# Kernel optimization log

Measured on AMD Instinct MI355X. Metric: run time of the kernel, lower is better.

## Reference

```python
import jax, jax.numpy as jnp
import numpy as np

N_NODES = 50000
N_EDGES = 800000
IN_CH = 512
HIDDEN = 512


def setup_inputs() -> dict:
    key = jax.random.key(0)
    k1, k2, k3, k4 = jax.random.split(key, 4)
    x = jax.random.normal(k1, (N_NODES, IN_CH), dtype=jnp.float32)
    edge_index = jax.random.randint(k2, (2, N_EDGES), 0, N_NODES, dtype=jnp.int64)
    # Glorot-style scaling for weights
    W1 = jax.random.normal(k3, (IN_CH, HIDDEN), dtype=jnp.float32) / np.sqrt(IN_CH)
    b1 = jnp.zeros((HIDDEN,), dtype=jnp.float32)
    W2 = jax.random.normal(k4, (HIDDEN, 1), dtype=jnp.float32) / np.sqrt(HIDDEN)
    b2 = jnp.zeros((1,), dtype=jnp.float32)
    return {"x": x, "edge_index": edge_index, "W1": W1, "b1": b1, "W2": W2, "b2": b2}


def _gcn_conv(x, edge_index, W, b):
    """PyG GCNConv: add self-loops, symmetric D^{-1/2}(A+I)D^{-1/2} normalization."""
    N = x.shape[0]
    xw = x @ W                                   # [N, out]
    row, col = edge_index[0], edge_index[1]      # source -> target
    # degree on target nodes, +1 for the self-loop
    deg = jax.ops.segment_sum(jnp.ones_like(col, dtype=xw.dtype), col, num_segments=N) + 1.0
    dis = jax.lax.rsqrt(deg)                     # deg^{-1/2}, [N]
    norm = dis[row] * dis[col]                   # [E]
    agg = jax.ops.segment_sum(norm[:, None] * xw[row], col, num_segments=N)
    agg = agg + (dis * dis)[:, None] * xw        # self-loop contribution
    return agg + b


def reference(x, edge_index, W1, b1, W2, b2):
    h = jax.nn.relu(_gcn_conv(x, edge_index, W1, b1))
    # dropout in eval mode (training=False) -> identity
    out = _gcn_conv(h, edge_index, W2, b2)
    return out.squeeze(-1)                       # [N]
```

## Files before the change

kernel.cpp:

```cpp
#include <hip/hip_runtime.h>

#define IN_CH 512
#define SCAN_BLK 1024

typedef _Float16 f16x8 __attribute__((ext_vector_type(8)));
typedef float f32x4 __attribute__((ext_vector_type(4)));

__device__ __forceinline__ void gload_lds16(const void* g, void* l) {
    __builtin_amdgcn_global_load_lds(
        (const __attribute__((address_space(1))) unsigned int*)g,
        (__attribute__((address_space(3))) unsigned int*)l, 16, 0, 0);
}

__global__ __launch_bounds__(256) void k_merged1(const float* __restrict__ W1,
                                                 _Float16* __restrict__ W1t,
                                                 const int* __restrict__ col,
                                                 int* __restrict__ deg, int E, int N) {
    __shared__ float tile[32][33];
    if ((int)blockIdx.x >= 256) {
        int e = ((int)blockIdx.x - 256) * 256 + threadIdx.x;
        if (e < E) {
            int d = col[e];
            if ((unsigned)d < (unsigned)N) atomicAdd(&deg[d], 1);
        }
        return;
    }
    const int bk = (blockIdx.x & 15) * 32, bn = (blockIdx.x >> 4) * 32;
    const int tx = threadIdx.x & 31, ty = threadIdx.x >> 5;
#pragma unroll
    for (int p = 0; p < 4; ++p)
        tile[ty + p * 8][tx] = W1[(size_t)(bk + ty + p * 8) * 512 + bn + tx];
    __syncthreads();
#pragma unroll
    for (int p = 0; p < 4; ++p)
        W1t[(size_t)(bn + ty + p * 8) * 512 + bk + tx] = (_Float16)tile[tx][ty + p * 8];
}

__global__ __launch_bounds__(SCAN_BLK) void k_psum(const int* __restrict__ deg,
                                                   int* __restrict__ bsum, int N) {
    __shared__ int red[SCAN_BLK / 64];
    int i = blockIdx.x * SCAN_BLK + threadIdx.x;
    int v = (i < N) ? deg[i] : 0;
#pragma unroll
    for (int off = 32; off > 0; off >>= 1) v += __shfl_down(v, off);
    if ((threadIdx.x & 63) == 0) red[threadIdx.x >> 6] = v;
    __syncthreads();
    if (threadIdx.x == 0) {
        int s = 0;
#pragma unroll
        for (int u = 0; u < SCAN_BLK / 64; ++u) s += red[u];
        bsum[blockIdx.x] = s;
    }
}

__global__ __launch_bounds__(SCAN_BLK) void k_write(const int* __restrict__ deg,
                                                    const int* __restrict__ bsum,
                                                    int* __restrict__ rp,
                                                    float* __restrict__ dis,
                                                    int* __restrict__ cursor, int N) {
    __shared__ int sums[SCAN_BLK];
    __shared__ int boff_s, tot_s;
    int t = threadIdx.x;
    if (t < 64) {
        int v = (t < (int)gridDim.x) ? bsum[t] : 0;
        int pre = (t < (int)blockIdx.x) ? v : 0;
        int a = pre, b = v;
#pragma unroll
        for (int off = 32; off > 0; off >>= 1) {
            a += __shfl_down(a, off);
            b += __shfl_down(b, off);
        }
        if (t == 0) { boff_s = a; tot_s = b; }
    }
    int i = blockIdx.x * SCAN_BLK + t;
    int d = (i < N) ? deg[i] : 0;
    sums[t] = d;
    __syncthreads();
    for (int off = 1; off < SCAN_BLK; off <<= 1) {
        int u = (t >= off) ? sums[t - off] : 0;
        __syncthreads();
        sums[t] += u;
        __syncthreads();
    }
    if (i < N) {
        rp[i] = boff_s + sums[t] - d;
        dis[i] = rsqrtf((float)d + 1.0f);
        cursor[i] = 0;
    }
    if (blockIdx.x == gridDim.x - 1 && t == 0) rp[N] = tot_s;
}

__global__ __launch_bounds__(256) void k_merged2(const float* __restrict__ A,
                                                 const _Float16* __restrict__ Bt,
                                                 _Float16* __restrict__ C,
                                                 int Nrows, int nbm, int nwg,
                                                 const int* __restrict__ ei,
                                                 const int* __restrict__ rp,
                                                 int* __restrict__ cursor,
                                                 int* __restrict__ csrc,
                                                 int E, int N) {
    __shared__ __align__(16) _Float16 As[128 * 64];
    __shared__ __align__(16) _Float16 Bs[128 * 64];

    if ((int)blockIdx.x >= nwg) {
        int e = ((int)blockIdx.x - nwg) * 256 + threadIdx.x;
        if (e < E) {
            int s = ei[e];
            int d = ei[E + e];
            if ((unsigned)s < (unsigned)N && (unsigned)d < (unsigned)N) {
                int pos = atomicAdd(&cursor[d], 1);
                csrc[rp[d] + pos] = s;
            }
        }
        return;
    }

    const int g = (int)blockIdx.x;
    const int t = threadIdx.x;
    const int lane = t & 63, w = t >> 6;
    const int wm = w >> 1, wn = w & 1;

    const int q = nwg >> 3, r = nwg & 7;
    const int xcd = g & 7, within = g >> 3;
    const int wg = (xcd < r ? xcd * (q + 1) : r * (q + 1) + (xcd - r) * q) + within;
    const int bm = (wg >> 2) * 128, bn = (wg & 3) * 128;

    const int rr = lane & 15, kg = lane >> 4;
    const int lrow = lane >> 3;
    const int scol = ((lane & 7) ^ lrow) * 8;
    const int rsw = rr & 7;
    const int arow = t >> 3;
    const int achk = t & 7;
    const int agcol = (achk ^ (arow & 7)) * 8;

    f32x4 acc[4][4];
#pragma unroll
    for (int i = 0; i < 4; ++i)
#pragma unroll
        for (int j = 0; j < 4; ++j) acc[i][j] = (f32x4)0.0f;

    for (int k0 = 0; k0 < 512; k0 += 64) {
#pragma unroll
        for (int p = 0; p < 4; ++p) {
            const int row = p * 32 + w * 8 + lrow;
            gload_lds16(Bt + (size_t)(bn + row) * 512 + k0 + scol,
                        Bs + (p * 32 + w * 8) * 64);
        }
#pragma unroll
        for (int p = 0; p < 4; ++p) {
            int grow = bm + p * 32 + arow;
            if (grow >= Nrows) grow = Nrows - 1;
            const float* gp = A + (size_t)grow * 512 + k0 + agcol;
            float4 u0 = *(const float4*)gp;
            float4 u1 = *(const float4*)(gp + 4);
            f16x8 o;
            o[0] = (_Float16)u0.x; o[1] = (_Float16)u0.y;
            o[2] = (_Float16)u0.z; o[3] = (_Float16)u0.w;
            o[4] = (_Float16)u1.x; o[5] = (_Float16)u1.y;
            o[6] = (_Float16)u1.z; o[7] = (_Float16)u1.w;
            *(f16x8*)(As + (p * 32 + arow) * 64 + achk * 8) = o;
        }
        __syncthreads();
#pragma unroll
        for (int kk = 0; kk < 2; ++kk) {
            f16x8 a[4], b[4];
#pragma unroll
            for (int i = 0; i < 4; ++i)
                a[i] = *(const f16x8*)(As + (wm * 64 + i * 16 + rr) * 64 +
                                       (((kk << 2) + kg) ^ rsw) * 8);
#pragma unroll
            for (int j = 0; j < 4; ++j)
                b[j] = *(const f16x8*)(Bs + (wn * 64 + j * 16 + rr) * 64 +
                                       (((kk << 2) + kg) ^ rsw) * 8);
#pragma unroll
            for (int i = 0; i < 4; ++i)
#pragma unroll
                for (int j = 0; j < 4; ++j)
                    acc[i][j] = __builtin_amdgcn_mfma_f32_16x16x32_f16(a[i], b[j], acc[i][j], 0, 0, 0);
        }
        __syncthreads();
    }

#pragma unroll
    for (int i = 0; i < 4; ++i)
#pragma unroll
        for (int j = 0; j < 4; ++j)
#pragma unroll
            for (int reg = 0; reg < 4; ++reg) {
                int m = bm + wm * 64 + i * 16 + kg * 4 + reg;
                int n = bn + wn * 64 + j * 16 + rr;
                C[(size_t)m * 512 + n] = (_Float16)acc[i][j][reg];
            }
}

__global__ __launch_bounds__(256) void k_agg(const _Float16* __restrict__ y,
                                             const float* __restrict__ dis,
                                             const int* __restrict__ rp,
                                             const int* __restrict__ csrc,
                                             const float* __restrict__ b1,
                                             const float* __restrict__ W2,
                                             float* __restrict__ z, int N) {
    const int n = blockIdx.x * 4 + (threadIdx.x >> 6);
    if (n >= N) return;
    const int l = threadIdx.x & 63;

    const float d1 = dis[n];
    f16x8 self = *(const f16x8*)(y + (size_t)n * 512 + l * 8);
    float acc[8];
#pragma unroll
    for (int c = 0; c < 8; ++c) acc[c] = d1 * (float)self[c];

    int j = rp[n], jend = rp[n + 1];
    for (; j + 8 <= jend; j += 8) {
        int s[8]; float wt[8]; f16x8 v[8];
#pragma unroll
        for (int u = 0; u < 8; ++u) s[u] = csrc[j + u];
#pragma unroll
        for (int u = 0; u < 8; ++u) wt[u] = dis[s[u]];
#pragma unroll
        for (int u = 0; u < 8; ++u)
            v[u] = *(const f16x8*)(y + (size_t)s[u] * 512 + l * 8);
#pragma unroll
        for (int u = 0; u < 8; ++u)
#pragma unroll
            for (int c = 0; c < 8; ++c) acc[c] += wt[u] * (float)v[u][c];
    }
    for (; j + 2 <= jend; j += 2) {
        int s0 = csrc[j], s1 = csrc[j + 1];
        float w0 = dis[s0], w1 = dis[s1];
        f16x8 v0 = *(const f16x8*)(y + (size_t)s0 * 512 + l * 8);
        f16x8 v1 = *(const f16x8*)(y + (size_t)s1 * 512 + l * 8);
#pragma unroll
        for (int c = 0; c < 8; ++c) acc[c] += w0 * (float)v0[c] + w1 * (float)v1[c];
    }
    if (j < jend) {
        int s0 = csrc[j];
        float w0 = dis[s0];
        f16x8 v0 = *(const f16x8*)(y + (size_t)s0 * 512 + l * 8);
#pragma unroll
        for (int c = 0; c < 8; ++c) acc[c] += w0 * (float)v0[c];
    }

    float4 bb0 = *(const float4*)(b1 + l * 8);
    float4 bb1 = *(const float4*)(b1 + l * 8 + 4);
    float4 w20 = *(const float4*)(W2 + l * 8);
    float4 w21 = *(const float4*)(W2 + l * 8 + 4);
    float bbv[8] = {bb0.x, bb0.y, bb0.z, bb0.w, bb1.x, bb1.y, bb1.z, bb1.w};
    float w2v[8] = {w20.x, w20.y, w20.z, w20.w, w21.x, w21.y, w21.z, w21.w};
    float p = 0.0f;
#pragma unroll
    for (int c = 0; c < 8; ++c) {
        float h = fmaxf(acc[c] * d1 + bbv[c], 0.0f);
        p += h * w2v[c];
    }
#pragma unroll
    for (int off = 32; off > 0; off >>= 1) p += __shfl_down(p, off);
    if (l == 0) z[n] = d1 * p;
}

__global__ void k_out(const float* __restrict__ z, const float* __restrict__ dis,
                      const int* __restrict__ rp, const int* __restrict__ csrc,
                      const float* __restrict__ b2, float* __restrict__ out, int N) {
    int n = blockIdx.x * blockDim.x + threadIdx.x;
    if (n >= N) return;
    float acc = z[n];
    int j = rp[n], jend = rp[n + 1];
    for (; j + 4 <= jend; j += 4) {
        float a0 = z[csrc[j]];
        float a1 = z[csrc[j + 1]];
        float a2 = z[csrc[j + 2]];
        float a3 = z[csrc[j + 3]];
        acc += (a0 + a1) + (a2 + a3);
    }
    for (; j < jend; ++j) acc += z[csrc[j]];
    out[n] = dis[n] * acc + b2[0];
}

extern "C" void kernel_launch(void* const* d_in, const int* in_sizes, int n_in,
                              void* d_out, int out_size, void* d_ws, size_t ws_size,
                              hipStream_t stream) {
    const float* x  = (const float*)d_in[0];
    const int*   ei = (const int*)d_in[1];
    const float* W1 = (const float*)d_in[2];
    const float* b1 = (const float*)d_in[3];
    const float* W2 = (const float*)d_in[4];
    const float* b2 = (const float*)d_in[5];
    float* out = (float*)d_out;

    const int N = in_sizes[0] / IN_CH;
    const int E = in_sizes[1] / 2;
    const int nbm = (N + 127) / 128;
    const int M2 = nbm * 128;
    const int NB = (N + SCAN_BLK - 1) / SCAN_BLK;
    const int DEGB = (E + 255) / 256;
    const int nwg  = nbm * 4;

    char* ws = (char*)d_ws;
    size_t off = 0;
    auto alloc = [&](size_t bytes) {
        char* p = ws + off;
        off += (bytes + 255) & ~(size_t)255;
        return p;
    };
    _Float16* y   = (_Float16*)alloc((size_t)M2 * 512 * sizeof(_Float16));
    _Float16* W1t = (_Float16*)alloc((size_t)512 * 512 * sizeof(_Float16));
    int*   deg    = (int*)alloc((size_t)N * sizeof(int));
    float* dis    = (float*)alloc((size_t)N * sizeof(float));
    int*   rp     = (int*)alloc((size_t)(N + 1) * sizeof(int));
    int*   cursor = (int*)alloc((size_t)N * sizeof(int));
    int*   csrc   = (int*)alloc((size_t)E * sizeof(int));
    float* z      = (float*)alloc((size_t)N * sizeof(float));
    int*   bsum   = (int*)alloc((size_t)64 * sizeof(int));

    hipMemsetAsync(deg, 0, (size_t)N * sizeof(int), stream);

    k_merged1<<<256 + DEGB, 256, 0, stream>>>(W1, W1t, ei + E, deg, E, N);
    k_psum<<<NB, SCAN_BLK, 0, stream>>>(deg, bsum, N);
    k_write<<<NB, SCAN_BLK, 0, stream>>>(deg, bsum, rp, dis, cursor, N);
    k_merged2<<<nwg + DEGB, 256, 0, stream>>>(x, W1t, y, N, nbm, nwg,
                                              ei, rp, cursor, csrc, E, N);
    k_agg<<<(N + 3) / 4, 256, 0, stream>>>(y, dis, rp, csrc, b1, W2, z, N);
    k_out<<<(N + 255) / 256, 256, 0, stream>>>(z, dis, rp, csrc, b2, out, N);
}
```

Before: 251.0 us.

## Prescale GEMM output by source degree norm and prefetch A tiles into registers

The GEMM epilogue now multiplies each output row by dis[m], so the stored features are already scaled by the source-side normalization. The aggregation kernel then just sums neighbour rows, dropping the per-edge dis[s] gather and multiply. The GEMM also loads the next A tile into registers before the MFMA loop so global loads overlap compute. The prefetch costs extra registers, and pre-scaling before the fp16 rounding slightly changes numerics.

```diff
diff --git a/kernel.cpp b/kernel.cpp
--- a/kernel.cpp
+++ b/kernel.cpp
@@ -92,6 +92,7 @@
 
 __global__ __launch_bounds__(256) void k_merged2(const float* __restrict__ A,
                                                  const _Float16* __restrict__ Bt,
+                                                 const float* __restrict__ dis,
                                                  _Float16* __restrict__ C,
                                                  int Nrows, int nbm, int nwg,
                                                  const int* __restrict__ ei,
@@ -133,6 +134,20 @@
     const int achk = t & 7;
     const int agcol = (achk ^ (arow & 7)) * 8;
 
+    const float* Abase[4];
+#pragma unroll
+    for (int p = 0; p < 4; ++p) {
+        int grow = bm + p * 32 + arow;
+        if (grow >= Nrows) grow = Nrows - 1;
+        Abase[p] = A + (size_t)grow * 512 + agcol;
+    }
+    float4 pa[4], pb[4];
+#pragma unroll
+    for (int p = 0; p < 4; ++p) {
+        pa[p] = *(const float4*)(Abase[p]);
+        pb[p] = *(const float4*)(Abase[p] + 4);
+    }
+
     f32x4 acc[4][4];
 #pragma unroll
     for (int i = 0; i < 4; ++i)
@@ -148,19 +163,21 @@
         }
 #pragma unroll
         for (int p = 0; p < 4; ++p) {
-            int grow = bm + p * 32 + arow;
-            if (grow >= Nrows) grow = Nrows - 1;
-            const float* gp = A + (size_t)grow * 512 + k0 + agcol;
-            float4 u0 = *(const float4*)gp;
-            float4 u1 = *(const float4*)(gp + 4);
             f16x8 o;
-            o[0] = (_Float16)u0.x; o[1] = (_Float16)u0.y;
-            o[2] = (_Float16)u0.z; o[3] = (_Float16)u0.w;
-            o[4] = (_Float16)u1.x; o[5] = (_Float16)u1.y;
-            o[6] = (_Float16)u1.z; o[7] = (_Float16)u1.w;
+            o[0] = (_Float16)pa[p].x; o[1] = (_Float16)pa[p].y;
+            o[2] = (_Float16)pa[p].z; o[3] = (_Float16)pa[p].w;
+            o[4] = (_Float16)pb[p].x; o[5] = (_Float16)pb[p].y;
+            o[6] = (_Float16)pb[p].z; o[7] = (_Float16)pb[p].w;
             *(f16x8*)(As + (p * 32 + arow) * 64 + achk * 8) = o;
         }
         __syncthreads();
+        if (k0 + 64 < 512) {
+#pragma unroll
+            for (int p = 0; p < 4; ++p) {
+                pa[p] = *(const float4*)(Abase[p] + k0 + 64);
+                pb[p] = *(const float4*)(Abase[p] + k0 + 68);
+            }
+        }
 #pragma unroll
         for (int kk = 0; kk < 2; ++kk) {
             f16x8 a[4], b[4];
@@ -184,13 +201,16 @@
 #pragma unroll
     for (int i = 0; i < 4; ++i)
 #pragma unroll
-        for (int j = 0; j < 4; ++j)
-#pragma unroll
-            for (int reg = 0; reg < 4; ++reg) {
-                int m = bm + wm * 64 + i * 16 + kg * 4 + reg;
+        for (int reg = 0; reg < 4; ++reg) {
+            int m = bm + wm * 64 + i * 16 + kg * 4 + reg;
+            int mc = (m < Nrows) ? m : Nrows - 1;
+            float dm = dis[mc];
+#pragma unroll
+            for (int j = 0; j < 4; ++j) {
                 int n = bn + wn * 64 + j * 16 + rr;
-                C[(size_t)m * 512 + n] = (_Float16)acc[i][j][reg];
+                C[(size_t)m * 512 + n] = (_Float16)(acc[i][j][reg] * dm);
             }
+        }
 }
 
 __global__ __launch_bounds__(256) void k_agg(const _Float16* __restrict__ y,
@@ -208,37 +228,32 @@
     f16x8 self = *(const f16x8*)(y + (size_t)n * 512 + l * 8);
     float acc[8];
 #pragma unroll
-    for (int c = 0; c < 8; ++c) acc[c] = d1 * (float)self[c];
+    for (int c = 0; c < 8; ++c) acc[c] = (float)self[c];
 
     int j = rp[n], jend = rp[n + 1];
     for (; j + 8 <= jend; j += 8) {
-        int s[8]; float wt[8]; f16x8 v[8];
+        int s[8]; f16x8 v[8];
 #pragma unroll
         for (int u = 0; u < 8; ++u) s[u] = csrc[j + u];
-#pragma unroll
-        for (int u = 0; u < 8; ++u) wt[u] = dis[s[u]];
 #pragma unroll
         for (int u = 0; u < 8; ++u)
             v[u] = *(const f16x8*)(y + (size_t)s[u] * 512 + l * 8);
 #pragma unroll
         for (int u = 0; u < 8; ++u)
 #pragma unroll
-            for (int c = 0; c < 8; ++c) acc[c] += wt[u] * (float)v[u][c];
+            for (int c = 0; c < 8; ++c) acc[c] += (float)v[u][c];
     }
     for (; j + 2 <= jend; j += 2) {
         int s0 = csrc[j], s1 = csrc[j + 1];
-        float w0 = dis[s0], w1 = dis[s1];
         f16x8 v0 = *(const f16x8*)(y + (size_t)s0 * 512 + l * 8);
         f16x8 v1 = *(const f16x8*)(y + (size_t)s1 * 512 + l * 8);
 #pragma unroll
-        for (int c = 0; c < 8; ++c) acc[c] += w0 * (float)v0[c] + w1 * (float)v1[c];
+        for (int c = 0; c < 8; ++c) acc[c] += (float)v0[c] + (float)v1[c];
     }
     if (j < jend) {
-        int s0 = csrc[j];
-        float w0 = dis[s0];
-        f16x8 v0 = *(const f16x8*)(y + (size_t)s0 * 512 + l * 8);
-#pragma unroll
-        for (int c = 0; c < 8; ++c) acc[c] += w0 * (float)v0[c];
+        f16x8 v0 = *(const f16x8*)(y + (size_t)csrc[j] * 512 + l * 8);
+#pragma unroll
+        for (int c = 0; c < 8; ++c) acc[c] += (float)v0[c];
     }
 
     float4 bb0 = *(const float4*)(b1 + l * 8);
@@ -317,7 +332,7 @@
     k_merged1<<<256 + DEGB, 256, 0, stream>>>(W1, W1t, ei + E, deg, E, N);
     k_psum<<<NB, SCAN_BLK, 0, stream>>>(deg, bsum, N);
     k_write<<<NB, SCAN_BLK, 0, stream>>>(deg, bsum, rp, dis, cursor, N);
-    k_merged2<<<nwg + DEGB, 256, 0, stream>>>(x, W1t, y, N, nbm, nwg,
+    k_merged2<<<nwg + DEGB, 256, 0, stream>>>(x, W1t, dis, y, N, nbm, nwg,
                                               ei, rp, cursor, csrc, E, N);
     k_agg<<<(N + 3) / 4, 256, 0, stream>>>(y, dis, rp, csrc, b1, W2, z, N);
     k_out<<<(N + 255) / 256, 256, 0, stream>>>(z, dis, rp, csrc, b2, out, N);
```

Result: no change. 246.7 us (-1.7%).
